# Optimization experiments

Measured on AMD Instinct MI355X. Metric: run time of the kernel, lower is better.

The kernel has to match this reference:

```python
import jax, jax.numpy as jnp
import numpy as np

B, N, H, NH = 2, 1024, 1024, 16  # batch, seq per branch, hidden, heads


def setup_inputs() -> dict:
    key = jax.random.key(0)
    k1, k2, k3, k4 = jax.random.split(key, 4)
    x = jax.random.normal(k1, (B, N, H), jnp.float32)
    x2 = jax.random.normal(k2, (B, N, H), jnp.float32)
    w_qkv = jax.random.normal(k3, (3 * H, H), jnp.float32) * 0.02  # nn.Linear(H, 3H), no bias
    w_out = jax.random.normal(k4, (H, H), jnp.float32) * 0.02
    b_out = jnp.zeros((H,), jnp.float32)
    return {"x": x, "x2": x2, "w_qkv": w_qkv, "w_out": w_out, "b_out": b_out, "num_heads": NH}


def _qkv_split(x, w_qkv, nh):
    # qkv Linear then Rearrange 'b n (qkv l d) -> qkv b l n d'
    b, n, h = x.shape
    d = h // nh
    qkv = x @ w_qkv.T                                    # [b, n, 3h]
    qkv = qkv.reshape(b, n, 3, nh, d).transpose(2, 0, 3, 1, 4)  # [3, b, nh, n, d]
    return qkv[0], qkv[1], qkv[2]


def reference(x, x2, w_qkv, w_out, b_out, num_heads):
    nh = num_heads
    d = x.shape[-1] // nh
    scale = float(d) ** -0.5
    q, k, v = _qkv_split(x, w_qkv, nh)
    q2, k2, v2 = _qkv_split(x2, w_qkv, nh)
    # cross-branch concat along seq dim
    q = jnp.concatenate([q, q2], axis=2)
    k = jnp.concatenate([k, k2], axis=2)
    v = jnp.concatenate([v, v2], axis=2)
    att = jax.nn.softmax(jnp.einsum('bhxd,bhyd->bhxy', q, k) * scale, axis=-1)  # [b,nh,2N,2N]
    o = jnp.einsum('bhxy,bhyd->bhxd', att, v)            # [b,nh,2N,d]
    o1, o2 = jnp.split(o, 2, axis=2)

    def proj(o):
        b, h, n, dd = o.shape
        o = o.transpose(0, 2, 1, 3).reshape(b, n, h * dd)  # 'b h l d -> b l (h d)'
        return o @ w_out.T + b_out

    return proj(o1), proj(o2)
```

## Files before the change

### kernel.cpp

```cpp
#include <hip/hip_runtime.h>
#include <hip/hip_bf16.h>

#define NB      2
#define NSEQ    1024
#define S2      2048
#define HDIM    1024
#define NHEADS  16
#define DHEAD   64
#define Q_SCALE 0.18033688011112042f

typedef unsigned short ushort_t;
typedef __attribute__((ext_vector_type(8))) short short8;
typedef __attribute__((ext_vector_type(4))) float f32x4;

__device__ __forceinline__ ushort_t f2bf(float f) {
    union { float f; unsigned int u; } c; c.f = f;
    unsigned int u = c.u;
    u += 0x7FFFu + ((u >> 16) & 1u);
    return (ushort_t)(u >> 16);
}

__device__ __forceinline__ unsigned pack_bf16x2(float a, float b) {
    union { __hip_bfloat162 h; unsigned u; } cv;
    cv.h = __float22bfloat162_rn(float2{a, b});
    return cv.u;
}

__global__ __launch_bounds__(256) void cvt_all(
    const float* __restrict__ x, const float* __restrict__ x2,
    const float* __restrict__ wqkv, const float* __restrict__ wout,
    ushort_t* __restrict__ Xb, ushort_t* __restrict__ Wqb, ushort_t* __restrict__ Wob)
{
    int b = blockIdx.x;
    const float* s; ushort_t* d; int i;
    if (b < 2048)      { s = x;    d = Xb;            i = b * 256 + threadIdx.x; }
    else if (b < 4096) { s = x2;   d = Xb + 2097152;  i = (b - 2048) * 256 + threadIdx.x; }
    else if (b < 7168) { s = wqkv; d = Wqb;           i = (b - 4096) * 256 + threadIdx.x; }
    else               { s = wout; d = Wob;           i = (b - 7168) * 256 + threadIdx.x; }
    float4 v = ((const float4*)s)[i];
    ushort4 o; o.x = f2bf(v.x); o.y = f2bf(v.y); o.z = f2bf(v.z); o.w = f2bf(v.w);
    ((ushort4*)d)[i] = o;
}

__global__ __launch_bounds__(256) void qkv_gemm_mfma(
    const ushort_t* __restrict__ Xb, const ushort_t* __restrict__ Wqb,
    ushort_t* __restrict__ Qb, ushort_t* __restrict__ Kb, ushort_t* __restrict__ Vtb)
{
    __shared__ ushort_t As[2 * 128 * 32];
    __shared__ ushort_t Bs[2 * 128 * 32];
    __shared__ float    Sc[4][16 * 20];
    const int t = threadIdx.x;
    const int lane = t & 63, quad = lane >> 4, l15 = lane & 15;
    const int w = t >> 6;
    const int wm = (w >> 1) * 64, wn = (w & 1) * 64;
    const int r0 = blockIdx.y * 128, c0 = blockIdx.x * 128;

    const int g_chunk = (lane & 3) ^ ((lane >> 3) & 3);
    const int srow_lo = w * 16 + (lane >> 2);

    auto stage = [&](int k0, int buf) {
        #pragma unroll
        for (int p = 0; p < 2; ++p) {
            int row = srow_lo + p * 64;
            const ushort_t* gpA = Xb  + (size_t)(r0 + row) * HDIM + k0 + g_chunk * 8;
            const ushort_t* gpB = Wqb + (size_t)(c0 + row) * HDIM + k0 + g_chunk * 8;
            ushort_t* lpA = As + buf * 4096 + p * 2048 + w * 512;
            ushort_t* lpB = Bs + buf * 4096 + p * 2048 + w * 512;
            __builtin_amdgcn_global_load_lds(
                (const __attribute__((address_space(1))) void*)gpA,
                (__attribute__((address_space(3))) void*)lpA, 16, 0, 0);
            __builtin_amdgcn_global_load_lds(
                (const __attribute__((address_space(1))) void*)gpB,
                (__attribute__((address_space(3))) void*)lpB, 16, 0, 0);
        }
    };

    f32x4 acc[4][4];
    #pragma unroll
    for (int i = 0; i < 4; ++i)
        #pragma unroll
        for (int j = 0; j < 4; ++j) acc[i][j] = (f32x4){0.f, 0.f, 0.f, 0.f};

    stage(0, 0);
    stage(32, 1);
    __syncthreads();

    const int sw = (l15 >> 1) & 3;
    for (int it = 0; it < 32; ++it) {
        const ushort_t* a = As + (it & 1) * 4096;
        const ushort_t* b = Bs + (it & 1) * 4096;
        short8 af[4], bf[4];
        #pragma unroll
        for (int mi = 0; mi < 4; ++mi) {
            int ra = wm + mi * 16 + l15;
            af[mi] = *(const short8*)(a + ra * 32 + ((quad ^ sw) * 8));
        }
        #pragma unroll
        for (int ni = 0; ni < 4; ++ni) {
            int rb = wn + ni * 16 + l15;
            bf[ni] = *(const short8*)(b + rb * 32 + ((quad ^ sw) * 8));
        }
        #pragma unroll
        for (int mi = 0; mi < 4; ++mi)
            #pragma unroll
            for (int ni = 0; ni < 4; ++ni)
                acc[mi][ni] = __builtin_amdgcn_mfma_f32_16x16x32_bf16(af[mi], bf[ni], acc[mi][ni], 0, 0, 0);
        __syncthreads();
        if (it < 30) stage((it + 2) * 32, it & 1);
    }

    const int branch = r0 >> 11;
    const int bb     = (r0 & 2047) >> 10;
    const int qi     = c0 >> 10;
    float* sc = &Sc[w][0];

    if (qi == 2) {
        #pragma unroll
        for (int mi = 0; mi < 4; ++mi) {
            int sbase = branch * NSEQ + (r0 & 1023) + wm + mi * 16 + quad * 4;
            #pragma unroll
            for (int ni = 0; ni < 4; ++ni) {
                int cc = (c0 & 1023) + wn + ni * 16;
                int h  = cc >> 6;
                int dd = (cc & 63) + l15;
                ushort4 pv;
                pv.x = f2bf(acc[mi][ni][0]); pv.y = f2bf(acc[mi][ni][1]);
                pv.z = f2bf(acc[mi][ni][2]); pv.w = f2bf(acc[mi][ni][3]);
                *(ushort4*)(Vtb + ((size_t)(bb * NHEADS + h) * DHEAD + dd) * S2 + sbase) = pv;
            }
        }
    } else {
        const float qsc = (qi == 0) ? Q_SCALE : 1.0f;
        ushort_t* base = (qi ? Kb : Qb);
        const int row = lane >> 2, ch = lane & 3;
        #pragma unroll
        for (int mi = 0; mi < 4; ++mi) {
            int sb = branch * NSEQ + (r0 & 1023) + wm + mi * 16;
            #pragma unroll
            for (int ni = 0; ni < 4; ++ni) {
                int cc = (c0 & 1023) + wn + ni * 16;
                int h  = cc >> 6;
                int db = cc & 63;
                #pragma unroll
                for (int reg = 0; reg < 4; ++reg)
                    sc[(quad * 4 + reg) * 20 + l15] = acc[mi][ni][reg] * qsc;
                float4 v = *(const float4*)&sc[row * 20 + ch * 4];
                uint2 pk;
                pk.x = pack_bf16x2(v.x, v.y);
                pk.y = pack_bf16x2(v.z, v.w);
                *(uint2*)(base + ((size_t)(bb * NHEADS + h) * S2 + sb + row) * DHEAD + db + ch * 4) = pk;
            }
        }
    }
}

__global__ __launch_bounds__(256) void attn_mfma(
    const ushort_t* __restrict__ Qb, const ushort_t* __restrict__ Kb,
    const ushort_t* __restrict__ Vtb, ushort_t* __restrict__ Ob)
{
    __shared__ ushort_t Ks[2][64 * 64];
    __shared__ ushort_t Vs[2][64 * 64];
    __shared__ ushort_t Ps[64][72];

    const int t = threadIdx.x, lane = t & 63, quad = lane >> 4, l15 = lane & 15, w = t >> 6;
    const int bh = blockIdx.z * NHEADS + blockIdx.y;
    const int r0 = blockIdx.x * 128;
    const ushort_t* Qh  = Qb  + (size_t)bh * S2 * DHEAD;
    const ushort_t* Kh  = Kb  + (size_t)bh * S2 * DHEAD;
    const ushort_t* Vth = Vtb + (size_t)bh * DHEAD * S2;

    const int slot = lane & 7;
    const int rsub = lane >> 3;
    auto prefetch = [&](int kt_, int buf_) {
        #pragma unroll
        for (int c = 0; c < 2; ++c) {
            int row = w * 16 + c * 8 + rsub;
            int gK  = slot ^ ((row >> 2) & 7);
            int gV  = slot ^ (row & 7);
            const ushort_t* gpK = Kh  + (size_t)(kt_ * 64 + row) * DHEAD + gK * 8;
            const ushort_t* gpV = Vth + (size_t)row * S2 + kt_ * 64 + gV * 8;
            ushort_t* lpK = &Ks[buf_][w * 1024 + c * 512];
            ushort_t* lpV = &Vs[buf_][w * 1024 + c * 512];
            __builtin_amdgcn_global_load_lds(
                (const __attribute__((address_space(1))) void*)gpK,
                (__attribute__((address_space(3))) void*)lpK, 16, 0, 0);
            __builtin_amdgcn_global_load_lds(
                (const __attribute__((address_space(1))) void*)gpV,
                (__attribute__((address_space(3))) void*)lpV, 16, 0, 0);
        }
    };

    short8 aq[2][2];
    #pragma unroll
    for (int s = 0; s < 2; ++s) {
        const int qrow = r0 + 32 * w + 16 * s + l15;
        aq[s][0] = *(const short8*)(Qh + (size_t)qrow * DHEAD + quad * 8);
        aq[s][1] = *(const short8*)(Qh + (size_t)qrow * DHEAD + 32 + quad * 8);
    }

    float lacc[2][4] = {};
    f32x4 oacc[2][4];
    #pragma unroll
    for (int s = 0; s < 2; ++s)
        #pragma unroll
        for (int nt = 0; nt < 4; ++nt) oacc[s][nt] = (f32x4){0.f, 0.f, 0.f, 0.f};

    prefetch(0, 0);
    prefetch(1, 1);
    __syncthreads();

    for (int kt = 0; kt < S2 / 64; ++kt) {
        const ushort_t* kb = &Ks[kt & 1][0];
        const ushort_t* vb = &Vs[kt & 1][0];

        short8 kf[4][2];
        #pragma unroll
        for (int nt = 0; nt < 4; ++nt) {
            const int key = 4 * l15 + nt;
            const ushort_t* krow = kb + key * 64;
            const int swz = l15 & 7;
            kf[nt][0] = *(const short8*)(krow + ((quad       ^ swz) * 8));
            kf[nt][1] = *(const short8*)(krow + (((4 + quad) ^ swz) * 8));
        }

        f32x4 sacc[2][4];
        #pragma unroll
        for (int s = 0; s < 2; ++s)
            #pragma unroll
            for (int nt = 0; nt < 4; ++nt) {
                f32x4 sv = (f32x4){0.f, 0.f, 0.f, 0.f};
                sv = __builtin_amdgcn_mfma_f32_16x16x32_bf16(aq[s][0], kf[nt][0], sv, 0, 0, 0);
                sv = __builtin_amdgcn_mfma_f32_16x16x32_bf16(aq[s][1], kf[nt][1], sv, 0, 0, 0);
                sacc[s][nt] = sv;
            }

        short8 vf[4][2];
        #pragma unroll
        for (int nt = 0; nt < 4; ++nt) {
            const int drow = nt * 16 + l15;
            vf[nt][0] = *(const short8*)(vb + drow * 64 + ((quad       ^ (drow & 7)) * 8));
            vf[nt][1] = *(const short8*)(vb + drow * 64 + (((4 + quad) ^ (drow & 7)) * 8));
        }

        #pragma unroll
        for (int s = 0; s < 2; ++s) {
            #pragma unroll
            for (int reg = 0; reg < 4; ++reg) {
                float p0 = __builtin_exp2f(sacc[s][0][reg]);
                float p1 = __builtin_exp2f(sacc[s][1][reg]);
                float p2 = __builtin_exp2f(sacc[s][2][reg]);
                float p3 = __builtin_exp2f(sacc[s][3][reg]);
                lacc[s][reg] += (p0 + p1) + (p2 + p3);
                uint2 pk;
                pk.x = pack_bf16x2(p0, p1);
                pk.y = pack_bf16x2(p2, p3);
                int prow = 16 * w + quad * 4 + reg;
                *(uint2*)&Ps[prow][4 * l15] = pk;
            }
            #pragma unroll
            for (int kk = 0; kk < 2; ++kk) {
                short8 pa = *(const short8*)&Ps[16 * w + l15][kk * 32 + quad * 8];
                #pragma unroll
                for (int nt = 0; nt < 4; ++nt)
                    oacc[s][nt] = __builtin_amdgcn_mfma_f32_16x16x32_bf16(pa, vf[nt][kk], oacc[s][nt], 0, 0, 0);
            }
        }

        __syncthreads();
        if (kt + 2 < S2 / 64) prefetch(kt + 2, kt & 1);
    }

    #pragma unroll
    for (int s = 0; s < 2; ++s)
        #pragma unroll
        for (int reg = 0; reg < 4; ++reg) {
            float l = lacc[s][reg];
            l += __shfl_xor(l, 1);
            l += __shfl_xor(l, 2);
            l += __shfl_xor(l, 4);
            l += __shfl_xor(l, 8);
            float inv = 1.f / l;
            size_t rowoff = ((size_t)bh * S2 + r0 + 32 * w + 16 * s + quad * 4 + reg) * DHEAD;
            #pragma unroll
            for (int nt = 0; nt < 4; ++nt)
                Ob[rowoff + nt * 16 + l15] = f2bf(oacc[s][nt][reg] * inv);
        }
}

__global__ __launch_bounds__(256) void proj_gemm_mfma(
    const ushort_t* __restrict__ Ob, const ushort_t* __restrict__ Wob,
    const float* __restrict__ Bo, float* __restrict__ Out)
{
    __shared__ ushort_t As[2 * 128 * 32];
    __shared__ ushort_t Bs[2 * 64 * 32];
    __shared__ float    Sc[4][16 * 20];
    const int t = threadIdx.x;
    const int lane = t & 63, quad = lane >> 4, l15 = lane & 15;
    const int w = t >> 6;
    const int wm = (w >> 1) * 64, wn = (w & 1) * 32;
    const int r0 = blockIdx.y * 128, c0 = blockIdx.x * 64;
    const int branch = r0 >> 11, bb = (r0 & 2047) >> 10;

    const int g_chunk = (lane & 3) ^ ((lane >> 3) & 3);
    const int srow_lo = w * 16 + (lane >> 2);

    auto stage = [&](int k0, int buf) {
        int h = k0 >> 6, off = k0 & 63;
        const ushort_t* gpB = Wob + (size_t)(c0 + srow_lo) * HDIM + k0 + g_chunk * 8;
        ushort_t* lpB = Bs + buf * 2048 + w * 512;
        __builtin_amdgcn_global_load_lds(
            (const __attribute__((address_space(1))) void*)gpB,
            (__attribute__((address_space(3))) void*)lpB, 16, 0, 0);
        #pragma unroll
        for (int p = 0; p < 2; ++p) {
            int row = srow_lo + p * 64;
            int s = branch * NSEQ + (r0 & 1023) + row;
            const ushort_t* gpA = Ob + ((size_t)(bb * NHEADS + h) * S2 + s) * DHEAD + off + g_chunk * 8;
            ushort_t* lpA = As + buf * 4096 + p * 2048 + w * 512;
            __builtin_amdgcn_global_load_lds(
                (const __attribute__((address_space(1))) void*)gpA,
                (__attribute__((address_space(3))) void*)lpA, 16, 0, 0);
        }
    };

    f32x4 acc[4][2];
    #pragma unroll
    for (int i = 0; i < 4; ++i)
        #pragma unroll
        for (int j = 0; j < 2; ++j) acc[i][j] = (f32x4){0.f, 0.f, 0.f, 0.f};

    stage(0, 0);
    stage(32, 1);
    __syncthreads();

    const int sw = (l15 >> 1) & 3;
    for (int it = 0; it < 32; ++it) {
        const ushort_t* a = As + (it & 1) * 4096;
        const ushort_t* b = Bs + (it & 1) * 2048;
        short8 af[4], bf[2];
        #pragma unroll
        for (int mi = 0; mi < 4; ++mi) {
            int ra = wm + mi * 16 + l15;
            af[mi] = *(const short8*)(a + ra * 32 + ((quad ^ sw) * 8));
        }
        #pragma unroll
        for (int ni = 0; ni < 2; ++ni) {
            int rb = wn + ni * 16 + l15;
            bf[ni] = *(const short8*)(b + rb * 32 + ((quad ^ sw) * 8));
        }
        #pragma unroll
        for (int mi = 0; mi < 4; ++mi)
            #pragma unroll
            for (int ni = 0; ni < 2; ++ni)
                acc[mi][ni] = __builtin_amdgcn_mfma_f32_16x16x32_bf16(af[mi], bf[ni], acc[mi][ni], 0, 0, 0);
        __syncthreads();
        if (it < 30) stage((it + 2) * 32, it & 1);
    }

    float* sc = &Sc[w][0];
    const int row = lane >> 2, ch = lane & 3;
    #pragma unroll
    for (int mi = 0; mi < 4; ++mi) {
        int rb0 = r0 + wm + mi * 16;
        #pragma unroll
        for (int ni = 0; ni < 2; ++ni) {
            int cb = c0 + wn + ni * 16;
            #pragma unroll
            for (int reg = 0; reg < 4; ++reg)
                sc[(quad * 4 + reg) * 20 + l15] = acc[mi][ni][reg];
            float4 v = *(const float4*)&sc[row * 20 + ch * 4];
            float4 bias = *(const float4*)&Bo[cb + ch * 4];
            v.x += bias.x; v.y += bias.y; v.z += bias.z; v.w += bias.w;
            *(float4*)&Out[(size_t)(rb0 + row) * HDIM + cb + ch * 4] = v;
        }
    }
}

extern "C" void kernel_launch(void* const* d_in, const int* in_sizes, int n_in,
                              void* d_out, int out_size, void* d_ws, size_t ws_size,
                              hipStream_t stream) {
    const float* x    = (const float*)d_in[0];
    const float* x2   = (const float*)d_in[1];
    const float* wqkv = (const float*)d_in[2];
    const float* wout = (const float*)d_in[3];
    const float* bout = (const float*)d_in[4];
    float* out = (float*)d_out;

    char* ws = (char*)d_ws;
    ushort_t* Xb  = (ushort_t*)(ws);
    ushort_t* Wqb = (ushort_t*)(ws + (8u  << 20));
    ushort_t* Wob = (ushort_t*)(ws + (14u << 20));
    ushort_t* Qb  = (ushort_t*)(ws + (16u << 20));
    ushort_t* Kb  = (ushort_t*)(ws + (24u << 20));
    ushort_t* Vtb = (ushort_t*)(ws + (32u << 20));
    ushort_t* Ob  = (ushort_t*)(ws + (40u << 20));

    cvt_all<<<8192, 256, 0, stream>>>(x, x2, wqkv, wout, Xb, Wqb, Wob);
    qkv_gemm_mfma<<<dim3(24, 32), 256, 0, stream>>>(Xb, Wqb, Qb, Kb, Vtb);
    attn_mfma<<<dim3(S2 / 128, NHEADS, NB), 256, 0, stream>>>(Qb, Kb, Vtb, Ob);
    proj_gemm_mfma<<<dim3(16, 32), 256, 0, stream>>>(Ob, Wob, bout, out);
}
```

Before: 212.4 us.

## Rewrite attention inner loop with 32x32x16 MFMA and register-resident P via permlane32 swap

```diff
diff --git a/kernel.cpp b/kernel.cpp
--- a/kernel.cpp
+++ b/kernel.cpp
@@ -12,6 +12,7 @@
 typedef unsigned short ushort_t;
 typedef __attribute__((ext_vector_type(8))) short short8;
 typedef __attribute__((ext_vector_type(4))) float f32x4;
+typedef __attribute__((ext_vector_type(16))) float f32x16;
 
 __device__ __forceinline__ ushort_t f2bf(float f) {
     union { float f; unsigned int u; } c; c.f = f;
@@ -160,9 +161,9 @@
 {
     __shared__ ushort_t Ks[2][64 * 64];
     __shared__ ushort_t Vs[2][64 * 64];
-    __shared__ ushort_t Ps[64][72];
-
-    const int t = threadIdx.x, lane = t & 63, quad = lane >> 4, l15 = lane & 15, w = t >> 6;
+
+    const int t = threadIdx.x, lane = t & 63, w = t >> 6;
+    const int l31 = lane & 31, hi = lane >> 5;
     const int bh = blockIdx.z * NHEADS + blockIdx.y;
     const int r0 = blockIdx.x * 128;
     const ushort_t* Qh  = Qb  + (size_t)bh * S2 * DHEAD;
@@ -175,10 +176,9 @@
         #pragma unroll
         for (int c = 0; c < 2; ++c) {
             int row = w * 16 + c * 8 + rsub;
-            int gK  = slot ^ ((row >> 2) & 7);
-            int gV  = slot ^ (row & 7);
-            const ushort_t* gpK = Kh  + (size_t)(kt_ * 64 + row) * DHEAD + gK * 8;
-            const ushort_t* gpV = Vth + (size_t)row * S2 + kt_ * 64 + gV * 8;
+            int g   = slot ^ (row & 7);
+            const ushort_t* gpK = Kh  + (size_t)(kt_ * 64 + row) * DHEAD + g * 8;
+            const ushort_t* gpV = Vth + (size_t)row * S2 + kt_ * 64 + g * 8;
             ushort_t* lpK = &Ks[buf_][w * 1024 + c * 512];
             ushort_t* lpV = &Vs[buf_][w * 1024 + c * 512];
             __builtin_amdgcn_global_load_lds(
@@ -190,101 +190,102 @@
         }
     };
 
-    short8 aq[2][2];
-    #pragma unroll
-    for (int s = 0; s < 2; ++s) {
-        const int qrow = r0 + 32 * w + 16 * s + l15;
-        aq[s][0] = *(const short8*)(Qh + (size_t)qrow * DHEAD + quad * 8);
-        aq[s][1] = *(const short8*)(Qh + (size_t)qrow * DHEAD + 32 + quad * 8);
-    }
-
-    float lacc[2][4] = {};
-    f32x4 oacc[2][4];
-    #pragma unroll
-    for (int s = 0; s < 2; ++s)
-        #pragma unroll
-        for (int nt = 0; nt < 4; ++nt) oacc[s][nt] = (f32x4){0.f, 0.f, 0.f, 0.f};
+    short8 aq[4];
+    {
+        const ushort_t* qp = Qh + (size_t)(r0 + 32 * w + l31) * DHEAD + hi * 8;
+        #pragma unroll
+        for (int sd = 0; sd < 4; ++sd) aq[sd] = *(const short8*)(qp + sd * 16);
+    }
+
+    const int s7 = l31 & 7;
+    int offA[4];
+    #pragma unroll
+    for (int s = 0; s < 4; ++s)
+        offA[s] = (l31 * 64 + (((s * 2 + hi) ^ s7) * 8)) * 2;
+
+    f32x16 oacc0, oacc1;
+    #pragma unroll
+    for (int i = 0; i < 16; ++i) { oacc0[i] = 0.f; oacc1[i] = 0.f; }
+    float la0 = 0.f, la1 = 0.f, la2 = 0.f, la3 = 0.f;
 
     prefetch(0, 0);
     prefetch(1, 1);
     __syncthreads();
 
     for (int kt = 0; kt < S2 / 64; ++kt) {
-        const ushort_t* kb = &Ks[kt & 1][0];
-        const ushort_t* vb = &Vs[kt & 1][0];
-
-        short8 kf[4][2];
-        #pragma unroll
-        for (int nt = 0; nt < 4; ++nt) {
-            const int key = 4 * l15 + nt;
-            const ushort_t* krow = kb + key * 64;
-            const int swz = l15 & 7;
-            kf[nt][0] = *(const short8*)(krow + ((quad       ^ swz) * 8));
-            kf[nt][1] = *(const short8*)(krow + (((4 + quad) ^ swz) * 8));
-        }
-
-        f32x4 sacc[2][4];
-        #pragma unroll
-        for (int s = 0; s < 2; ++s)
-            #pragma unroll
-            for (int nt = 0; nt < 4; ++nt) {
-                f32x4 sv = (f32x4){0.f, 0.f, 0.f, 0.f};
-                sv = __builtin_amdgcn_mfma_f32_16x16x32_bf16(aq[s][0], kf[nt][0], sv, 0, 0, 0);
-                sv = __builtin_amdgcn_mfma_f32_16x16x32_bf16(aq[s][1], kf[nt][1], sv, 0, 0, 0);
-                sacc[s][nt] = sv;
+        const char* kb = (const char*)&Ks[kt & 1][0];
+        const char* vb = (const char*)&Vs[kt & 1][0];
+
+        f32x16 s0, s1;
+        #pragma unroll
+        for (int i = 0; i < 16; ++i) { s0[i] = 0.f; s1[i] = 0.f; }
+        __builtin_amdgcn_s_setprio(1);
+        #pragma unroll
+        for (int sd = 0; sd < 4; ++sd) {
+            short8 k0 = *(const short8*)(kb + offA[sd]);
+            short8 k1 = *(const short8*)(kb + offA[sd] + 4096);
+            s0 = __builtin_amdgcn_mfma_f32_32x32x16_bf16(k0, aq[sd], s0, 0, 0, 0);
+            s1 = __builtin_amdgcn_mfma_f32_32x32x16_bf16(k1, aq[sd], s1, 0, 0, 0);
+        }
+        __builtin_amdgcn_s_setprio(0);
+
+        unsigned pw[4][4];
+        #pragma unroll
+        for (int half = 0; half < 2; ++half) {
+            float p[8], q[8];
+            #pragma unroll
+            for (int j = 0; j < 8; ++j) {
+                p[j] = __builtin_exp2f(s0[half * 8 + j]);
+                q[j] = __builtin_exp2f(s1[half * 8 + j]);
             }
-
-        short8 vf[4][2];
-        #pragma unroll
-        for (int nt = 0; nt < 4; ++nt) {
-            const int drow = nt * 16 + l15;
-            vf[nt][0] = *(const short8*)(vb + drow * 64 + ((quad       ^ (drow & 7)) * 8));
-            vf[nt][1] = *(const short8*)(vb + drow * 64 + (((4 + quad) ^ (drow & 7)) * 8));
-        }
-
-        #pragma unroll
-        for (int s = 0; s < 2; ++s) {
-            #pragma unroll
-            for (int reg = 0; reg < 4; ++reg) {
-                float p0 = __builtin_exp2f(sacc[s][0][reg]);
-                float p1 = __builtin_exp2f(sacc[s][1][reg]);
-                float p2 = __builtin_exp2f(sacc[s][2][reg]);
-                float p3 = __builtin_exp2f(sacc[s][3][reg]);
-                lacc[s][reg] += (p0 + p1) + (p2 + p3);
-                uint2 pk;
-                pk.x = pack_bf16x2(p0, p1);
-                pk.y = pack_bf16x2(p2, p3);
-                int prow = 16 * w + quad * 4 + reg;
-                *(uint2*)&Ps[prow][4 * l15] = pk;
-            }
-            #pragma unroll
-            for (int kk = 0; kk < 2; ++kk) {
-                short8 pa = *(const short8*)&Ps[16 * w + l15][kk * 32 + quad * 8];
-                #pragma unroll
-                for (int nt = 0; nt < 4; ++nt)
-                    oacc[s][nt] = __builtin_amdgcn_mfma_f32_16x16x32_bf16(pa, vf[nt][kk], oacc[s][nt], 0, 0, 0);
-            }
-        }
+            la0 += p[0] + p[4]; la1 += p[1] + p[5];
+            la2 += p[2] + p[6]; la3 += p[3] + p[7];
+            la0 += q[0] + q[4]; la1 += q[1] + q[5];
+            la2 += q[2] + q[6]; la3 += q[3] + q[7];
+
+            unsigned a0 = pack_bf16x2(p[0], p[1]), b0 = pack_bf16x2(p[2], p[3]);
+            unsigned c0 = pack_bf16x2(p[4], p[5]), d0 = pack_bf16x2(p[6], p[7]);
+            asm("v_permlane32_swap_b32 %0, %1" : "+v"(a0), "+v"(c0));
+            asm("v_permlane32_swap_b32 %0, %1" : "+v"(b0), "+v"(d0));
+            pw[half][0] = a0; pw[half][1] = b0; pw[half][2] = c0; pw[half][3] = d0;
+
+            unsigned a1 = pack_bf16x2(q[0], q[1]), b1 = pack_bf16x2(q[2], q[3]);
+            unsigned c1 = pack_bf16x2(q[4], q[5]), d1 = pack_bf16x2(q[6], q[7]);
+            asm("v_permlane32_swap_b32 %0, %1" : "+v"(a1), "+v"(c1));
+            asm("v_permlane32_swap_b32 %0, %1" : "+v"(b1), "+v"(d1));
+            pw[2 + half][0] = a1; pw[2 + half][1] = b1; pw[2 + half][2] = c1; pw[2 + half][3] = d1;
+        }
+
+        __builtin_amdgcn_s_setprio(1);
+        #pragma unroll
+        for (int sk = 0; sk < 4; ++sk) {
+            union { unsigned u[4]; short8 s8; } pa;
+            pa.u[0] = pw[sk][0]; pa.u[1] = pw[sk][1];
+            pa.u[2] = pw[sk][2]; pa.u[3] = pw[sk][3];
+            short8 v0 = *(const short8*)(vb + offA[sk]);
+            short8 v1 = *(const short8*)(vb + offA[sk] + 4096);
+            oacc0 = __builtin_amdgcn_mfma_f32_32x32x16_bf16(pa.s8, v0, oacc0, 0, 0, 0);
+            oacc1 = __builtin_amdgcn_mfma_f32_32x32x16_bf16(pa.s8, v1, oacc1, 0, 0, 0);
+        }
+        __builtin_amdgcn_s_setprio(0);
 
         __syncthreads();
         if (kt + 2 < S2 / 64) prefetch(kt + 2, kt & 1);
     }
 
-    #pragma unroll
-    for (int s = 0; s < 2; ++s)
-        #pragma unroll
-        for (int reg = 0; reg < 4; ++reg) {
-            float l = lacc[s][reg];
-            l += __shfl_xor(l, 1);
-            l += __shfl_xor(l, 2);
-            l += __shfl_xor(l, 4);
-            l += __shfl_xor(l, 8);
-            float inv = 1.f / l;
-            size_t rowoff = ((size_t)bh * S2 + r0 + 32 * w + 16 * s + quad * 4 + reg) * DHEAD;
-            #pragma unroll
-            for (int nt = 0; nt < 4; ++nt)
-                Ob[rowoff + nt * 16 + l15] = f2bf(oacc[s][nt][reg] * inv);
-        }
+    float l = (la0 + la1) + (la2 + la3);
+    l += __shfl_xor(l, 32);
+    const float inv = 1.0f / l;
+
+    ushort_t* obase = Ob + (size_t)bh * S2 * DHEAD;
+    #pragma unroll
+    for (int r = 0; r < 16; ++r) {
+        const int ql = (r & 3) + 8 * (r >> 2) + 4 * hi;
+        const float iv = __shfl(inv, ql);
+        const size_t rowoff = (size_t)(r0 + 32 * w + ql) * DHEAD;
+        obase[rowoff + l31]      = f2bf(oacc0[r] * iv);
+        obase[rowoff + 32 + l31] = f2bf(oacc1[r] * iv);
+    }
 }
 
 __global__ __launch_bounds__(256) void proj_gemm_mfma(
```

Measured after the change: 212.7 us. No clear change (+0.1%).
